# Kernel optimization log

Hardware: AMD Instinct MI355X
Metric: run time of the kernel (lower is better)

Reference implementation:

```python
import jax, jax.numpy as jnp
import numpy as np

B, S, D, H = 2, 2048, 1024, 16  # batch, seq, embed_dim, num_heads
DH = D // H                      # head dim = 64


def setup_inputs() -> dict:
    key = jax.random.key(0)
    kx, kq, kbq, kk, kbk, kv, kbv = jax.random.split(key, 7)
    scale = 1.0 / np.sqrt(D)
    return {
        "x": jax.random.normal(kx, (B, S, D), dtype=jnp.float32),
        "Wq": jax.random.normal(kq, (D, D), dtype=jnp.float32) * scale,
        "bq": jax.random.normal(kbq, (D,), dtype=jnp.float32) * 0.01,
        "Wk": jax.random.normal(kk, (D, D), dtype=jnp.float32) * scale,
        "bk": jax.random.normal(kbk, (D,), dtype=jnp.float32) * 0.01,
        "Wv": jax.random.normal(kv, (D, D), dtype=jnp.float32) * scale,
        "bv": jax.random.normal(kbv, (D,), dtype=jnp.float32) * 0.01,
    }


def reference(x, Wq, bq, Wk, bk, Wv, bv):
    # ooqkv_type == 'q', odeint_method == 'id': q branch = act(Linear(x)), exact GELU (torch nn.GELU default)
    q = jax.nn.gelu(x @ Wq + bq, approximate=False)
    k = x @ Wk + bk
    v = x @ Wv + bv
    # [B, S, D] -> [B, S, H, DH]
    q = q.reshape(B, S, H, DH)
    k = k.reshape(B, S, H, DH)
    v = v.reshape(B, S, H, DH)
    # NOTE: original module has NO 1/sqrt(d) scale — faithful reproduction
    att = jnp.einsum("bqhd,bkhd->bhqk", q, k)
    att = jax.nn.softmax(att, axis=-1)
    out = jnp.einsum("bhqk,bkhd->bqhd", att, v)
    return out.reshape(B, S, D)
```

## Files before the change

### kernel.cpp

```cpp
#include <hip/hip_runtime.h>
#include <math.h>

#define B_  2
#define S_  2048
#define D_  1024
#define H_  16
#define DH_ 64
#define M_  (B_ * S_)

typedef _Float16 half_t;
typedef __attribute__((ext_vector_type(8))) _Float16 h8;
typedef __attribute__((ext_vector_type(4))) _Float16 h4;
typedef __attribute__((ext_vector_type(4))) float   f32x4;

#define LOG2E 1.44269504088896f

__device__ __forceinline__ void gll16(const half_t* g, half_t* l) {
    __builtin_amdgcn_global_load_lds(
        (__attribute__((address_space(1))) const void*)g,
        (__attribute__((address_space(3))) void*)l, 16, 0, 0);
}

__global__ __launch_bounds__(256) void prep_k(
    const float* __restrict__ x, half_t* __restrict__ xh,
    const float* __restrict__ Wq, const float* __restrict__ Wk,
    const float* __restrict__ Wv, half_t* __restrict__ Wt)
{
    const int bx = blockIdx.x;
    if (bx < 2048) {
        const size_t i = ((size_t)bx * 256 + threadIdx.x) * 8;
        const float4 a = *(const float4*)(x + i);
        const float4 b = *(const float4*)(x + i + 4);
        h8 o;
        o[0] = (half_t)a.x; o[1] = (half_t)a.y; o[2] = (half_t)a.z; o[3] = (half_t)a.w;
        o[4] = (half_t)b.x; o[5] = (half_t)b.y; o[6] = (half_t)b.z; o[7] = (half_t)b.w;
        *(h8*)(xh + i) = o;
    } else {
        const int gb    = bx - 2048;
        const int which = gb >> 9;
        const float* __restrict__ W = (which == 0) ? Wq : (which == 1) ? Wk : Wv;
        half_t* __restrict__ T = Wt + (size_t)which * D_ * D_;
        const int gw   = (gb & 511) * 4 + (threadIdx.x >> 6);
        const int lane = threadIdx.x & 63;
        const int n    = (gw & 15) * 64 + lane;
        const int k0   = (gw >> 4) * 8;
        h8 o;
        #pragma unroll
        for (int t = 0; t < 8; ++t) o[t] = (half_t)W[(size_t)(k0 + t) * D_ + n];
        *(h8*)(T + (size_t)n * D_ + k0) = o;
    }
}

__global__ __launch_bounds__(512) void qkv_gemm_f16(
    const half_t* __restrict__ xh, const half_t* __restrict__ Wt,
    const float* __restrict__ bq, const float* __restrict__ bk,
    const float* __restrict__ bv,
    half_t* __restrict__ Qo, half_t* __restrict__ Ko, half_t* __restrict__ Vt)
{
    const int lin = blockIdx.y * 24 + blockIdx.x;
    const int xcd = lin & 7;
    const int idx = lin >> 3;
    const int n0g = (xcd * 3 + idx % 3) * 128;
    const int m0  = (idx / 3) * 128;
    const int which = n0g >> 10;
    const int n0    = n0g & 1023;
    const half_t* __restrict__ Wp  = Wt + (size_t)which * D_ * D_;
    const float* __restrict__ bias = (which == 0) ? bq : (which == 1) ? bk : bv;

    const int tid = threadIdx.x, lane = tid & 63, wave = tid >> 6;
    const int wm = (wave & 3) * 32, wn = (wave >> 2) * 64;
    const int ln = lane & 15, quad = lane >> 4;

    __shared__ __align__(16) half_t SMEM[128 * 136];
    half_t* const As = SMEM;
    half_t* const Bs = SMEM + 128 * 64;

    const int r0  = tid >> 3, c0 = tid & 7;
    const int cs  = c0 ^ (r0 & 7);
    const half_t* aS = xh + (size_t)(m0 + r0) * D_ + cs * 8;
    const half_t* bS = Wp + (size_t)(n0 + r0) * D_ + cs * 8;

    f32x4 acc[2][4];
    #pragma unroll
    for (int i = 0; i < 2; ++i)
        #pragma unroll
        for (int j = 0; j < 4; ++j) acc[i][j] = (f32x4){0.f, 0.f, 0.f, 0.f};

    for (int k0 = 0; k0 < D_; k0 += 64) {
        __syncthreads();
        gll16(aS,            &As[tid * 8]);
        gll16(aS + 64 * D_,  &As[(tid + 512) * 8]);
        gll16(bS,            &Bs[tid * 8]);
        gll16(bS + 64 * D_,  &Bs[(tid + 512) * 8]);
        aS += 64; bS += 64;
        __syncthreads();

        #pragma unroll
        for (int kc = 0; kc < 2; ++kc) {
            h8 af[2], bf[4];
            #pragma unroll
            for (int i = 0; i < 2; ++i) {
                const int r = wm + i * 16 + ln;
                af[i] = *(const h8*)&As[r * 64 + (((kc << 2) + quad) ^ (r & 7)) * 8];
            }
            #pragma unroll
            for (int j = 0; j < 4; ++j) {
                const int r = wn + j * 16 + ln;
                bf[j] = *(const h8*)&Bs[r * 64 + (((kc << 2) + quad) ^ (r & 7)) * 8];
            }
            #pragma unroll
            for (int i = 0; i < 2; ++i)
                #pragma unroll
                for (int j = 0; j < 4; ++j)
                    acc[i][j] = __builtin_amdgcn_mfma_f32_16x16x32_f16(
                        af[i], bf[j], acc[i][j], 0, 0, 0);
        }
    }

    if (which == 2) {
        #pragma unroll
        for (int j = 0; j < 4; ++j) {
            const int col = n0 + wn + j * 16 + ln;
            const int h = col >> 6, d = col & 63;
            const float bb = bias[col];
            #pragma unroll
            for (int i = 0; i < 2; ++i) {
                const int sg = m0 + wm + i * 16 + quad * 4;
                const int b  = sg >> 11, srow = sg & 2047;
                h4 pv;
                #pragma unroll
                for (int r = 0; r < 4; ++r) pv[r] = (half_t)(acc[i][j][r] + bb);
                *(h4*)(Vt + (((size_t)(b * H_ + h) * DH_ + d) * S_ + srow)) = pv;
            }
        }
    } else {
        half_t* __restrict__ outp = (which == 0) ? Qo : Ko;
        __syncthreads();
        #pragma unroll
        for (int j = 0; j < 4; ++j) {
            const int col = wn + j * 16 + ln;
            const float bb = bias[n0 + col];
            #pragma unroll
            for (int i = 0; i < 2; ++i) {
                #pragma unroll
                for (int r = 0; r < 4; ++r) {
                    const int row = wm + i * 16 + quad * 4 + r;
                    float t = acc[i][j][r] + bb;
                    if (which == 0) {
                        const float u = t * fmaf(t * t, 0.0356774081f, 0.7978845608f);
                        const float e = __builtin_amdgcn_exp2f(u * -2.88539008178f);
                        t = t * __builtin_amdgcn_rcpf(1.0f + e) * LOG2E;
                    }
                    SMEM[row * 136 + col] = (half_t)t;
                }
            }
        }
        __syncthreads();
        const int cc = tid & 15;
        const int rr = tid >> 4;
        #pragma unroll
        for (int p = 0; p < 4; ++p) {
            const int row = p * 32 + rr;
            const h8 v = *(const h8*)&SMEM[row * 136 + cc * 8];
            *(h8*)(outp + (size_t)(m0 + row) * D_ + n0 + cc * 8) = v;
        }
    }
}

#define DEFER_THR 10.0f
#define ATTN_TILE(KS, VS)                                                     \
    do {                                                                      \
        f32x4 sa[4];                                                          \
        __builtin_amdgcn_s_setprio(1);                                        \
        _Pragma("unroll")                                                     \
        for (int j = 0; j < 4; ++j) {                                         \
            const int rK = j * 16 + ln;                                       \
            const h8 ka0 = *(const h8*)&KS[rK * 64 + ((quad)     ^ (rK & 7)) * 8]; \
            const h8 ka1 = *(const h8*)&KS[rK * 64 + ((quad + 4) ^ (rK & 7)) * 8]; \
            f32x4 t = (f32x4){0.f, 0.f, 0.f, 0.f};                            \
            t = __builtin_amdgcn_mfma_f32_16x16x32_f16(ka0, qa0, t, 0, 0, 0); \
            t = __builtin_amdgcn_mfma_f32_16x16x32_f16(ka1, qa1, t, 0, 0, 0); \
            sa[j] = t;                                                        \
        }                                                                     \
        __builtin_amdgcn_s_setprio(0);                                        \
        float mj[4];                                                          \
        _Pragma("unroll")                                                     \
        for (int j = 0; j < 4; ++j)                                           \
            mj[j] = fmaxf(fmaxf(sa[j][0], sa[j][1]),                          \
                          fmaxf(sa[j][2], sa[j][3]));                         \
        float mxa = fmaxf(fmaxf(mj[0], mj[1]), fmaxf(mj[2], mj[3]));          \
        mxa = fmaxf(mxa, __shfl_xor(mxa, 16, 64));                            \
        mxa = fmaxf(mxa, __shfl_xor(mxa, 32, 64));                            \
        if (__ballot(mxa > m_a + DEFER_THR)) {                                \
            const float mna = fmaxf(m_a, mxa);                                \
            const float ala = __builtin_amdgcn_exp2f(m_a - mna);              \
            m_a = mna;                                                        \
            float ra[4];                                                      \
            _Pragma("unroll")                                                 \
            for (int r = 0; r < 4; ++r) ra[r] = __shfl(ala, quad * 4 + r, 64);\
            _Pragma("unroll")                                                 \
            for (int r = 0; r < 4; ++r) {                                     \
                la[r] *= ra[r];                                               \
                _Pragma("unroll")                                             \
                for (int j = 0; j < 4; ++j) Oa[j][r] *= ra[r];                \
            }                                                                 \
        }                                                                     \
        _Pragma("unroll")                                                     \
        for (int j = 0; j < 4; ++j) {                                         \
            h4 pva;                                                           \
            _Pragma("unroll")                                                 \
            for (int r = 0; r < 4; ++r)                                       \
                pva[r] = (half_t)__builtin_amdgcn_exp2f(sa[j][r] - m_a);      \
            *(h4*)&QPs[wave * 16 + ln][j * 16 + quad * 4] = pva;              \
        }                                                                     \
        const h8 pa0 = *(const h8*)&QPs[wave * 16 + ln][quad * 8];            \
        const h8 pa1 = *(const h8*)&QPs[wave * 16 + ln][32 + quad * 8];       \
        __builtin_amdgcn_s_setprio(1);                                        \
        _Pragma("unroll")                                                     \
        for (int j = 0; j < 4; ++j) {                                         \
            const int rV = j * 16 + ln;                                       \
            const h8 vb0 = *(const h8*)&VS[rV * 64 + ((quad)     ^ (rV & 7)) * 8]; \
            const h8 vb1 = *(const h8*)&VS[rV * 64 + ((quad + 4) ^ (rV & 7)) * 8]; \
            Oa[j] = __builtin_amdgcn_mfma_f32_16x16x32_f16(pa0, vb0, Oa[j], 0, 0, 0); \
            Oa[j] = __builtin_amdgcn_mfma_f32_16x16x32_f16(pa1, vb1, Oa[j], 0, 0, 0); \
        }                                                                     \
        la = __builtin_amdgcn_mfma_f32_16x16x32_f16(pa0, ones8, la, 0, 0, 0); \
        la = __builtin_amdgcn_mfma_f32_16x16x32_f16(pa1, ones8, la, 0, 0, 0); \
        __builtin_amdgcn_s_setprio(0);                                        \
    } while (0)

__global__ __launch_bounds__(512) void attn_f16(
    const half_t* __restrict__ Q, const half_t* __restrict__ K,
    const half_t* __restrict__ Vt, float* __restrict__ out)
{
    const int tid  = threadIdx.x;
    const int lane = tid & 63;
    const int wave = tid >> 6;
    const int ln   = lane & 15;
    const int quad = lane >> 4;

    const int lin = blockIdx.y * 16 + blockIdx.x;
    const int swz = (lin & 7) * 64 + (lin >> 3);
    const int bh  = swz >> 4;
    const int b   = bh >> 4;
    const int h   = bh & 15;
    const int q0  = (swz & 15) * 128;

    const half_t* __restrict__ Qb  = Q  + (size_t)b * S_ * D_ + h * DH_;
    const half_t* __restrict__ Kb  = K  + (size_t)b * S_ * D_ + h * DH_;
    const half_t* __restrict__ Vtb = Vt + (size_t)bh * DH_ * S_;

    __shared__ __align__(16) half_t Ks0[64 * 64];
    __shared__ __align__(16) half_t Vs0[64 * 64];
    __shared__ __align__(16) half_t Ks1[64 * 64];
    __shared__ __align__(16) half_t Vs1[64 * 64];
    __shared__ __align__(16) half_t QPs[128][72];

    const int sr  = tid >> 3, sc0 = tid & 7;
    const int scs = sc0 ^ (sr & 7);
    const half_t* kS = Kb  + (size_t)sr * D_ + scs * 8;
    const half_t* vS = Vtb + (size_t)sr * S_ + scs * 8;
    half_t* const kD0 = &Ks0[tid * 8];
    half_t* const vD0 = &Vs0[tid * 8];
    half_t* const kD1 = &Ks1[tid * 8];
    half_t* const vD1 = &Vs1[tid * 8];

    gll16(kS, kD0); gll16(vS, vD0);
    kS += 64 * D_; vS += 64;

    #pragma unroll
    for (int l = 0; l < 2; ++l) {
        const int c = tid + l * 512;
        const int r = c >> 3, k8 = c & 7;
        *(h8*)&QPs[r][k8 * 8] = *(const h8*)(Qb + (size_t)(q0 + r) * D_ + k8 * 8);
    }
    __syncthreads();
    const h8 qa0 = *(const h8*)&QPs[wave * 16 + ln][quad * 8];
    const h8 qa1 = *(const h8*)&QPs[wave * 16 + ln][32 + quad * 8];

    h8 ones8;
    #pragma unroll
    for (int t = 0; t < 8; ++t) ones8[t] = (half_t)1.0f;

    f32x4 Oa[4];
    #pragma unroll
    for (int j = 0; j < 4; ++j) Oa[j] = (f32x4){0.f, 0.f, 0.f, 0.f};
    f32x4 la = (f32x4){0.f, 0.f, 0.f, 0.f};
    float m_a = -INFINITY;

    for (int it = 0; it < 16; ++it) {
        gll16(kS, kD1); gll16(vS, vD1);
        kS += 64 * D_; vS += 64;
        ATTN_TILE(Ks0, Vs0);
        __syncthreads();

        if (it < 15) {
            gll16(kS, kD0); gll16(vS, vD0);
            kS += 64 * D_; vS += 64;
        }
        ATTN_TILE(Ks1, Vs1);
        __syncthreads();
    }

    #pragma unroll
    for (int r = 0; r < 4; ++r) {
        const float iva = 1.0f / la[r];
        const int rowa = q0 + wave * 16 + quad * 4 + r;
        #pragma unroll
        for (int j = 0; j < 4; ++j)
            out[((size_t)b * S_ + rowa) * D_ + h * DH_ + j * 16 + ln] = Oa[j][r] * iva;
    }
}

extern "C" void kernel_launch(void* const* d_in, const int* in_sizes, int n_in,
                              void* d_out, int out_size, void* d_ws, size_t ws_size,
                              hipStream_t stream) {
    const float* x  = (const float*)d_in[0];
    const float* Wq = (const float*)d_in[1];
    const float* bq = (const float*)d_in[2];
    const float* Wk = (const float*)d_in[3];
    const float* bk = (const float*)d_in[4];
    const float* Wv = (const float*)d_in[5];
    const float* bv = (const float*)d_in[6];
    float* out = (float*)d_out;

    const size_t nmd = (size_t)M_ * D_;
    const size_t ndd = (size_t)D_ * D_;
    half_t* xh  = (half_t*)d_ws;
    half_t* Wt  = xh + nmd;
    half_t* Qh  = Wt + 3 * ndd;
    half_t* Kh  = Qh + nmd;
    half_t* Vtw = Kh + nmd;

    prep_k<<<2048 + 1536, 256, 0, stream>>>(x, xh, Wq, Wk, Wv, Wt);
    qkv_gemm_f16<<<dim3(3 * D_ / 128, M_ / 128), 512, 0, stream>>>(
        xh, Wt, bq, bk, bv, Qh, Kh, Vtw);
    attn_f16<<<dim3(S_ / 128, B_ * H_), 512, 0, stream>>>(Qh, Kh, Vtw, out);
}
```

Measured before the change: 177.2 us.

## Split attention KV range across two blocks and merge with combine kernel

Attention now splits the key/value sequence into two halves via a third grid dimension, doubling the block count from 512 to 1024 so the GPU's compute units are better filled. Each half writes a normalized partial output plus its row max and row sum, and a new combine kernel merges them with log-sum-exp weights. The aim is to fix under-occupancy of the attention grid, at the cost of an extra kernel launch, extra global traffic for the partial outputs, and fp16 rounding of the second half's partial. Workspace buffers from earlier stages are reused for the partials.

Result: slower. 190.0 us (+7.2%).

```diff
diff --git a/kernel.cpp b/kernel.cpp
--- a/kernel.cpp
+++ b/kernel.cpp
@@ -231,13 +231,17 @@
 
 __global__ __launch_bounds__(512) void attn_f16(
     const half_t* __restrict__ Q, const half_t* __restrict__ K,
-    const half_t* __restrict__ Vt, float* __restrict__ out)
+    const half_t* __restrict__ Vt, float* __restrict__ out,
+    half_t* __restrict__ O1,
+    float* __restrict__ m0a, float* __restrict__ l0a,
+    float* __restrict__ m1a, float* __restrict__ l1a)
 {
     const int tid  = threadIdx.x;
     const int lane = tid & 63;
     const int wave = tid >> 6;
     const int ln   = lane & 15;
     const int quad = lane >> 4;
+    const int half = blockIdx.z;
 
     const int lin = blockIdx.y * 16 + blockIdx.x;
     const int swz = (lin & 7) * 64 + (lin >> 3);
@@ -258,8 +262,8 @@
 
     const int sr  = tid >> 3, sc0 = tid & 7;
     const int scs = sc0 ^ (sr & 7);
-    const half_t* kS = Kb  + (size_t)sr * D_ + scs * 8;
-    const half_t* vS = Vtb + (size_t)sr * S_ + scs * 8;
+    const half_t* kS = Kb  + (size_t)(half * 1024 + sr) * D_ + scs * 8;
+    const half_t* vS = Vtb + (size_t)sr * S_ + half * 1024 + scs * 8;
     half_t* const kD0 = &Ks0[tid * 8];
     half_t* const vD0 = &Vs0[tid * 8];
     half_t* const kD1 = &Ks1[tid * 8];
@@ -288,13 +292,13 @@
     f32x4 la = (f32x4){0.f, 0.f, 0.f, 0.f};
     float m_a = -INFINITY;
 
-    for (int it = 0; it < 16; ++it) {
+    for (int it = 0; it < 8; ++it) {
         gll16(kS, kD1); gll16(vS, vD1);
         kS += 64 * D_; vS += 64;
         ATTN_TILE(Ks0, Vs0);
         __syncthreads();
 
-        if (it < 15) {
+        if (it < 7) {
             gll16(kS, kD0); gll16(vS, vD0);
             kS += 64 * D_; vS += 64;
         }
@@ -302,13 +306,70 @@
         __syncthreads();
     }
 
+    if (half == 0) {
+        #pragma unroll
+        for (int r = 0; r < 4; ++r) {
+            const float iva = 1.0f / la[r];
+            const int rowa = q0 + wave * 16 + quad * 4 + r;
+            #pragma unroll
+            for (int j = 0; j < 4; ++j)
+                out[((size_t)b * S_ + rowa) * D_ + h * DH_ + j * 16 + ln] =
+                    Oa[j][r] * iva;
+        }
+        if (lane < 16) m0a[bh * S_ + q0 + wave * 16 + lane] = m_a;
+        if (ln == 0) {
+            #pragma unroll
+            for (int r = 0; r < 4; ++r)
+                l0a[bh * S_ + q0 + wave * 16 + quad * 4 + r] = la[r];
+        }
+    } else {
+        #pragma unroll
+        for (int r = 0; r < 4; ++r) {
+            const float iva = 1.0f / la[r];
+            const int rowa = q0 + wave * 16 + quad * 4 + r;
+            #pragma unroll
+            for (int j = 0; j < 4; ++j)
+                O1[((size_t)b * S_ + rowa) * D_ + h * DH_ + j * 16 + ln] =
+                    (half_t)(Oa[j][r] * iva);
+        }
+        if (lane < 16) m1a[bh * S_ + q0 + wave * 16 + lane] = m_a;
+        if (ln == 0) {
+            #pragma unroll
+            for (int r = 0; r < 4; ++r)
+                l1a[bh * S_ + q0 + wave * 16 + quad * 4 + r] = la[r];
+        }
+    }
+}
+
+__global__ __launch_bounds__(256) void combine_k(
+    float* __restrict__ out, const half_t* __restrict__ O1,
+    const float* __restrict__ m0a, const float* __restrict__ l0a,
+    const float* __restrict__ m1a, const float* __restrict__ l1a)
+{
+    const int t = blockIdx.x * 256 + threadIdx.x;
+    const size_t e0 = (size_t)t * 16;
+    const int h   = (int)((e0 >> 6) & 15);
+    const int s   = (int)((e0 >> 10) & 2047);
+    const int b   = (int)(e0 >> 21);
+    const int rid = ((b * 16 + h) << 11) | s;
+    const float m0 = m0a[rid], l0 = l0a[rid];
+    const float m1 = m1a[rid], l1 = l1a[rid];
+    const float M  = fmaxf(m0, m1);
+    const float w0 = l0 * __builtin_amdgcn_exp2f(m0 - M);
+    const float w1 = l1 * __builtin_amdgcn_exp2f(m1 - M);
+    const float inv = 1.0f / (w0 + w1);
+    const float a0 = w0 * inv, a1 = w1 * inv;
+    float4* po = (float4*)(out + e0);
+    const h4* p1 = (const h4*)(O1 + e0);
     #pragma unroll
-    for (int r = 0; r < 4; ++r) {
-        const float iva = 1.0f / la[r];
-        const int rowa = q0 + wave * 16 + quad * 4 + r;
-        #pragma unroll
-        for (int j = 0; j < 4; ++j)
-            out[((size_t)b * S_ + rowa) * D_ + h * DH_ + j * 16 + ln] = Oa[j][r] * iva;
+    for (int k = 0; k < 4; ++k) {
+        float4 v = po[k];
+        const h4 o1v = p1[k];
+        v.x = v.x * a0 + (float)o1v[0] * a1;
+        v.y = v.y * a0 + (float)o1v[1] * a1;
+        v.z = v.z * a0 + (float)o1v[2] * a1;
+        v.w = v.w * a0 + (float)o1v[3] * a1;
+        po[k] = v;
     }
 }
 
@@ -332,8 +393,16 @@
     half_t* Kh  = Qh + nmd;
     half_t* Vtw = Kh + nmd;
 
+    half_t* O1  = xh;
+    float*  m0a = (float*)Wt;
+    float*  l0a = m0a + 65536;
+    float*  m1a = l0a + 65536;
+    float*  l1a = m1a + 65536;
+
     prep_k<<<2048 + 1536, 256, 0, stream>>>(x, xh, Wq, Wk, Wv, Wt);
     qkv_gemm_f16<<<dim3(3 * D_ / 128, M_ / 128), 512, 0, stream>>>(
         xh, Wt, bq, bk, bv, Qh, Kh, Vtw);
-    attn_f16<<<dim3(S_ / 128, B_ * H_), 512, 0, stream>>>(Qh, Kh, Vtw, out);
-}
+    attn_f16<<<dim3(S_ / 128, B_ * H_, 2), 512, 0, stream>>>(
+        Qh, Kh, Vtw, out, O1, m0a, l0a, m1a, l1a);
+    combine_k<<<1024, 256, 0, stream>>>(out, O1, m0a, l0a, m1a, l1a);
+}
```
